# Kernel optimization log

Hardware: AMD Instinct MI355X
Metric: run time of the kernel (lower is better)

Reference implementation:

```python
import jax, jax.numpy as jnp
import numpy as np
import math

# ---- HashGridEncoder constants (from init_kwargs) ----
L = 16            # levels
LOG2T = 19
T = 1 << LOG2T    # hash table size per level
F = 2             # features per entry
N_MIN = 16
N_MAX = 2048
N_PTS = 524288    # number of query points
BB_MIN = np.zeros(3, np.float32)
BB_MAX = np.ones(3, np.float32)
B = math.exp((math.log(N_MAX) - math.log(N_MIN)) / (L - 1))
RES = np.array([math.floor(N_MIN * B ** i) for i in range(L)], dtype=np.float32)  # per-level grid resolution
VERTS = np.array([[0,0,0],[0,0,1],[0,1,0],[0,1,1],[1,0,0],[1,0,1],[1,1,0],[1,1,1]], dtype=np.int32)  # 8 cube corners
PI = np.array([1, 2654435761, 805459861], dtype=np.uint32)  # spatial hash primes
MASK = np.uint32((1 << 19) - 1)  # hard-coded mask from source


def setup_inputs() -> dict:
    key = jax.random.key(0)
    k1, k2 = jax.random.split(key)
    xyz = jax.random.uniform(k1, (N_PTS, 3), dtype=jnp.float32)  # points inside bbox [0,1]^3
    # nn.init.uniform_(weight, -1e-4, 1e-4)
    tables = jax.random.uniform(k2, (L, T, F), minval=-1e-4, maxval=1e-4, dtype=jnp.float32)
    return {"xyz": xyz, "tables": tables}


def reference(xyz, tables):
    # cell size per level: (bb_max - bb_min) / resolution  -> [L,3]
    cell = (BB_MAX - BB_MIN)[None, :] / RES[:, None]
    # normalized grid coords for all levels at once: [L,N,3]
    u = (xyz[None, :, :] - BB_MIN) / cell[:, None, :]
    mi = jnp.floor(u).astype(jnp.int32)            # min corner index [L,N,3]
    d = u - mi.astype(jnp.float32)                 # trilinear fracs == (xyz - min_vertex)/cell, [L,N,3]
    # 8 corner integer coords: [L,N,8,3]; uint32 wrapping matches int64-mul + low-19-bit mask
    corners = (mi[:, :, None, :] + VERTS[None, None]).astype(jnp.uint32)
    h = (corners[..., 0] * PI[0]) ^ (corners[..., 1] * PI[1]) ^ (corners[..., 2] * PI[2])
    h = (h & MASK).astype(jnp.int32)               # hash indices [L,N,8], all < T
    # gather all levels in one flat lookup
    flat = tables.reshape(L * T, F)
    idx = h + (jnp.arange(L, dtype=jnp.int32) * T)[:, None, None]
    emb = flat[idx]                                # [L,N,8,F]
    # trilinear weights: prod over axes of d (corner bit 1) or 1-d (corner bit 0) -> [L,N,8]
    w = jnp.prod(jnp.where(VERTS[None, None].astype(bool), d[:, :, None, :], 1.0 - d[:, :, None, :]), axis=-1)
    c = jnp.einsum('lnv,lnvf->lnf', w, emb)        # interpolated features [L,N,F]
    # torch.cat(embedded, dim=-1): level-major concat -> [N, L*F]
    return jnp.moveaxis(c, 0, 1).reshape(xyz.shape[0], L * F)
```

## Files before the change

kernel.cpp:

```cpp
#include <hip/hip_runtime.h>
#include <cmath>

#define NLEVELS 16
#define TBL     (1u << 19)
#define HMASK   0x7FFFFu
#define NPTS    524288
#define NCHUNK  (NPTS / 256)

typedef float v4f __attribute__((ext_vector_type(4)));

struct LevelParams {
    float cell[NLEVELS];
};

__device__ __forceinline__ float2 level_interp(
    float x, float y, float z, float cell,
    const float2* __restrict__ tab)
{
    const float ux = x / cell;
    const float uy = y / cell;
    const float uz = z / cell;
    const float fx = floorf(ux);
    const float fy = floorf(uy);
    const float fz = floorf(uz);
    const float dx = ux - fx;
    const float dy = uy - fy;
    const float dz = uz - fz;

    const unsigned ix = (unsigned)(int)fx;
    const unsigned iy = (unsigned)(int)fy;
    const unsigned iz = (unsigned)(int)fz;

    const unsigned hx0 = ix;
    const unsigned hx1 = ix + 1u;
    const unsigned hy0 = iy * 2654435761u;
    const unsigned hy1 = (iy + 1u) * 2654435761u;
    const unsigned hz0 = iz * 805459861u;
    const unsigned hz1 = (iz + 1u) * 805459861u;

    const unsigned h0 = (hx0 ^ hy0 ^ hz0) & HMASK;
    const unsigned h1 = (hx0 ^ hy0 ^ hz1) & HMASK;
    const unsigned h2 = (hx0 ^ hy1 ^ hz0) & HMASK;
    const unsigned h3 = (hx0 ^ hy1 ^ hz1) & HMASK;
    const unsigned h4 = (hx1 ^ hy0 ^ hz0) & HMASK;
    const unsigned h5 = (hx1 ^ hy0 ^ hz1) & HMASK;
    const unsigned h6 = (hx1 ^ hy1 ^ hz0) & HMASK;
    const unsigned h7 = (hx1 ^ hy1 ^ hz1) & HMASK;

    const float2 e0 = tab[h0];
    const float2 e1 = tab[h1];
    const float2 e2 = tab[h2];
    const float2 e3 = tab[h3];
    const float2 e4 = tab[h4];
    const float2 e5 = tab[h5];
    const float2 e6 = tab[h6];
    const float2 e7 = tab[h7];

    const float wx0 = 1.0f - dx;
    const float wy0 = 1.0f - dy;
    const float wz0 = 1.0f - dz;

    const float p00 = wx0 * wy0;
    const float p01 = wx0 * dy;
    const float p10 = dx * wy0;
    const float p11 = dx * dy;

    const float w0 = p00 * wz0;
    const float w1 = p00 * dz;
    const float w2 = p01 * wz0;
    const float w3 = p01 * dz;
    const float w4 = p10 * wz0;
    const float w5 = p10 * dz;
    const float w6 = p11 * wz0;
    const float w7 = p11 * dz;

    float c0 = w0 * e0.x;
    float c1 = w0 * e0.y;
    c0 += w1 * e1.x;  c1 += w1 * e1.y;
    c0 += w2 * e2.x;  c1 += w2 * e2.y;
    c0 += w3 * e3.x;  c1 += w3 * e3.y;
    c0 += w4 * e4.x;  c1 += w4 * e4.y;
    c0 += w5 * e5.x;  c1 += w5 * e5.y;
    c0 += w6 * e6.x;  c1 += w6 * e6.y;
    c0 += w7 * e7.x;  c1 += w7 * e7.y;

    return make_float2(c0, c1);
}

__global__ __launch_bounds__(256) void ngp_phase1(
    const float* __restrict__ xyz,
    const float* __restrict__ tables,
    float2* __restrict__ ws,
    LevelParams lp)
{
    const unsigned b = blockIdx.x;
    const int level = (int)(((b >> 14) << 3) | (b & 7u));
    const int chunk = (int)((b >> 3) & (NCHUNK - 1u));
    const int n = chunk * 256 + threadIdx.x;

    const float x = xyz[3 * n + 0];
    const float y = xyz[3 * n + 1];
    const float z = xyz[3 * n + 2];

    const float cell = lp.cell[level];
    const float2* __restrict__ tab = (const float2*)tables + ((size_t)level << 19);

    const float2 c = level_interp(x, y, z, cell, tab);

    ws[(size_t)level * NPTS + n] = c;
}

__global__ __launch_bounds__(256) void ngp_phase2(
    const float2* __restrict__ ws,
    float* __restrict__ out)
{
    const unsigned j = blockIdx.x * 256 + threadIdx.x;
    const unsigned n = j >> 3;
    const unsigned k = j & 7u;

    const float2 a = ws[(size_t)(2u * k)      * NPTS + n];
    const float2 b = ws[(size_t)(2u * k + 1u) * NPTS + n];

    v4f v = { a.x, a.y, b.x, b.y };
    *(v4f*)(out + (size_t)j * 4) = v;
}

__global__ __launch_bounds__(256) void ngp_encode(
    const float* __restrict__ xyz,
    const float* __restrict__ tables,
    float* __restrict__ out,
    LevelParams lp)
{
    const int n = blockIdx.x * 256 + threadIdx.x;
    const float x = xyz[3 * n + 0];
    const float y = xyz[3 * n + 1];
    const float z = xyz[3 * n + 2];

    float acc[2 * NLEVELS];
    const float2* __restrict__ tab_base = (const float2*)tables;

    #pragma unroll
    for (int l = 0; l < NLEVELS; ++l) {
        const float2 c = level_interp(x, y, z, lp.cell[l],
                                      tab_base + ((size_t)l << 19));
        acc[2 * l + 0] = c.x;
        acc[2 * l + 1] = c.y;
    }

    v4f* o4 = (v4f*)(out + (size_t)n * 32);
    #pragma unroll
    for (int j = 0; j < 8; ++j) {
        v4f v = { acc[4 * j + 0], acc[4 * j + 1],
                  acc[4 * j + 2], acc[4 * j + 3] };
        o4[j] = v;
    }
}

extern "C" void kernel_launch(void* const* d_in, const int* in_sizes, int n_in,
                              void* d_out, int out_size, void* d_ws, size_t ws_size,
                              hipStream_t stream) {
    const float* xyz    = (const float*)d_in[0];
    const float* tables = (const float*)d_in[1];
    float* out          = (float*)d_out;

    LevelParams lp;
    const double B = std::exp((std::log(2048.0) - std::log(16.0)) / 15.0);
    for (int i = 0; i < NLEVELS; ++i) {
        const double r = std::floor(16.0 * std::pow(B, (double)i));
        lp.cell[i] = 1.0f / (float)r;
    }

    const size_t ws_needed = (size_t)NLEVELS * NPTS * sizeof(float2);

    if (ws_size >= ws_needed) {
        float2* ws = (float2*)d_ws;
        hipLaunchKernelGGL(ngp_phase1, dim3(NLEVELS * NCHUNK), dim3(256), 0, stream,
                           xyz, tables, ws, lp);
        hipLaunchKernelGGL(ngp_phase2, dim3(NPTS * 8 / 256), dim3(256), 0, stream,
                           ws, out);
    } else {
        hipLaunchKernelGGL(ngp_encode, dim3(NPTS / 256), dim3(256), 0, stream,
                           xyz, tables, out, lp);
    }
}
```

Before: 381.1 us.

## Process two points per thread in phase1 and transpose phase2 via LDS

Phase1 now has each thread handle two points, issuing all 16 gathers before combining, to raise memory-level parallelism and halve the block count. Phase2 stages each block's 256 points times 16 levels in padded shared memory, then writes fully contiguous output rows. This replaces scattered strided reads with coalesced loads. The cost is higher register pressure in phase1 and an LDS round trip plus barrier in phase2.

```diff
diff --git a/kernel.cpp b/kernel.cpp
--- a/kernel.cpp
+++ b/kernel.cpp
@@ -5,7 +5,6 @@
 #define TBL     (1u << 19)
 #define HMASK   0x7FFFFu
 #define NPTS    524288
-#define NCHUNK  (NPTS / 256)
 
 typedef float v4f __attribute__((ext_vector_type(4)));
 
@@ -13,9 +12,9 @@
     float cell[NLEVELS];
 };
 
-__device__ __forceinline__ float2 level_interp(
-    float x, float y, float z, float cell,
-    const float2* __restrict__ tab)
+__device__ __forceinline__ void ngp_hash(
+    float x, float y, float z, float cell, unsigned* __restrict__ h,
+    float& dx, float& dy, float& dz)
 {
     const float ux = x / cell;
     const float uy = y / cell;
@@ -23,9 +22,9 @@
     const float fx = floorf(ux);
     const float fy = floorf(uy);
     const float fz = floorf(uz);
-    const float dx = ux - fx;
-    const float dy = uy - fy;
-    const float dz = uz - fz;
+    dx = ux - fx;
+    dy = uy - fy;
+    dz = uz - fz;
 
     const unsigned ix = (unsigned)(int)fx;
     const unsigned iy = (unsigned)(int)fy;
@@ -38,52 +37,46 @@
     const unsigned hz0 = iz * 805459861u;
     const unsigned hz1 = (iz + 1u) * 805459861u;
 
-    const unsigned h0 = (hx0 ^ hy0 ^ hz0) & HMASK;
-    const unsigned h1 = (hx0 ^ hy0 ^ hz1) & HMASK;
-    const unsigned h2 = (hx0 ^ hy1 ^ hz0) & HMASK;
-    const unsigned h3 = (hx0 ^ hy1 ^ hz1) & HMASK;
-    const unsigned h4 = (hx1 ^ hy0 ^ hz0) & HMASK;
-    const unsigned h5 = (hx1 ^ hy0 ^ hz1) & HMASK;
-    const unsigned h6 = (hx1 ^ hy1 ^ hz0) & HMASK;
-    const unsigned h7 = (hx1 ^ hy1 ^ hz1) & HMASK;
-
-    const float2 e0 = tab[h0];
-    const float2 e1 = tab[h1];
-    const float2 e2 = tab[h2];
-    const float2 e3 = tab[h3];
-    const float2 e4 = tab[h4];
-    const float2 e5 = tab[h5];
-    const float2 e6 = tab[h6];
-    const float2 e7 = tab[h7];
-
+    h[0] = (hx0 ^ hy0 ^ hz0) & HMASK;
+    h[1] = (hx0 ^ hy0 ^ hz1) & HMASK;
+    h[2] = (hx0 ^ hy1 ^ hz0) & HMASK;
+    h[3] = (hx0 ^ hy1 ^ hz1) & HMASK;
+    h[4] = (hx1 ^ hy0 ^ hz0) & HMASK;
+    h[5] = (hx1 ^ hy0 ^ hz1) & HMASK;
+    h[6] = (hx1 ^ hy1 ^ hz0) & HMASK;
+    h[7] = (hx1 ^ hy1 ^ hz1) & HMASK;
+}
+
+__device__ __forceinline__ void ngp_weights(
+    float dx, float dy, float dz, float* __restrict__ w)
+{
     const float wx0 = 1.0f - dx;
     const float wy0 = 1.0f - dy;
     const float wz0 = 1.0f - dz;
-
     const float p00 = wx0 * wy0;
     const float p01 = wx0 * dy;
     const float p10 = dx * wy0;
     const float p11 = dx * dy;
-
-    const float w0 = p00 * wz0;
-    const float w1 = p00 * dz;
-    const float w2 = p01 * wz0;
-    const float w3 = p01 * dz;
-    const float w4 = p10 * wz0;
-    const float w5 = p10 * dz;
-    const float w6 = p11 * wz0;
-    const float w7 = p11 * dz;
-
-    float c0 = w0 * e0.x;
-    float c1 = w0 * e0.y;
-    c0 += w1 * e1.x;  c1 += w1 * e1.y;
-    c0 += w2 * e2.x;  c1 += w2 * e2.y;
-    c0 += w3 * e3.x;  c1 += w3 * e3.y;
-    c0 += w4 * e4.x;  c1 += w4 * e4.y;
-    c0 += w5 * e5.x;  c1 += w5 * e5.y;
-    c0 += w6 * e6.x;  c1 += w6 * e6.y;
-    c0 += w7 * e7.x;  c1 += w7 * e7.y;
-
+    w[0] = p00 * wz0;
+    w[1] = p00 * dz;
+    w[2] = p01 * wz0;
+    w[3] = p01 * dz;
+    w[4] = p10 * wz0;
+    w[5] = p10 * dz;
+    w[6] = p11 * wz0;
+    w[7] = p11 * dz;
+}
+
+__device__ __forceinline__ float2 ngp_combine(
+    const float* __restrict__ w, const float2* __restrict__ e)
+{
+    float c0 = w[0] * e[0].x;
+    float c1 = w[0] * e[0].y;
+    #pragma unroll
+    for (int c = 1; c < 8; ++c) {
+        c0 += w[c] * e[c].x;
+        c1 += w[c] * e[c].y;
+    }
     return make_float2(c0, c1);
 }
 
@@ -94,35 +87,69 @@
     LevelParams lp)
 {
     const unsigned b = blockIdx.x;
-    const int level = (int)(((b >> 14) << 3) | (b & 7u));
-    const int chunk = (int)((b >> 3) & (NCHUNK - 1u));
-    const int n = chunk * 256 + threadIdx.x;
-
-    const float x = xyz[3 * n + 0];
-    const float y = xyz[3 * n + 1];
-    const float z = xyz[3 * n + 2];
+    const int level = (int)(((b >> 13) << 3) | (b & 7u));
+    const int chunk = (int)((b >> 3) & 1023u);
+    const int n0 = chunk * 512 + threadIdx.x;
+    const int n1 = n0 + 256;
+
+    const float x0 = xyz[3 * n0 + 0];
+    const float y0 = xyz[3 * n0 + 1];
+    const float z0 = xyz[3 * n0 + 2];
+    const float x1 = xyz[3 * n1 + 0];
+    const float y1 = xyz[3 * n1 + 1];
+    const float z1 = xyz[3 * n1 + 2];
 
     const float cell = lp.cell[level];
     const float2* __restrict__ tab = (const float2*)tables + ((size_t)level << 19);
 
-    const float2 c = level_interp(x, y, z, cell, tab);
-
-    ws[(size_t)level * NPTS + n] = c;
-}
+    unsigned h0[8], h1[8];
+    float dx0, dy0, dz0, dx1, dy1, dz1;
+    ngp_hash(x0, y0, z0, cell, h0, dx0, dy0, dz0);
+    ngp_hash(x1, y1, z1, cell, h1, dx1, dy1, dz1);
+
+    float2 e0[8], e1[8];
+    #pragma unroll
+    for (int c = 0; c < 8; ++c) e0[c] = tab[h0[c]];
+    #pragma unroll
+    for (int c = 0; c < 8; ++c) e1[c] = tab[h1[c]];
+
+    float w0[8], w1[8];
+    ngp_weights(dx0, dy0, dz0, w0);
+    ngp_weights(dx1, dy1, dz1, w1);
+
+    const float2 r0 = ngp_combine(w0, e0);
+    const float2 r1 = ngp_combine(w1, e1);
+
+    ws[(size_t)level * NPTS + n0] = r0;
+    ws[(size_t)level * NPTS + n1] = r1;
+}
+
+#define P2STRIDE 258
 
 __global__ __launch_bounds__(256) void ngp_phase2(
     const float2* __restrict__ ws,
     float* __restrict__ out)
 {
-    const unsigned j = blockIdx.x * 256 + threadIdx.x;
-    const unsigned n = j >> 3;
-    const unsigned k = j & 7u;
-
-    const float2 a = ws[(size_t)(2u * k)      * NPTS + n];
-    const float2 b = ws[(size_t)(2u * k + 1u) * NPTS + n];
-
-    v4f v = { a.x, a.y, b.x, b.y };
-    *(v4f*)(out + (size_t)j * 4) = v;
+    __shared__ float2 lds[NLEVELS * P2STRIDE];
+    const unsigned base = blockIdx.x * 256;
+    const unsigned tid = threadIdx.x;
+
+    #pragma unroll
+    for (int l = 0; l < NLEVELS; ++l)
+        lds[l * P2STRIDE + tid] = ws[(size_t)l * NPTS + base + tid];
+
+    __syncthreads();
+
+    #pragma unroll
+    for (int it = 0; it < 8; ++it) {
+        const unsigned j = it * 256 + tid;
+        const unsigned nl = j >> 3;
+        const unsigned k = j & 7u;
+        const float2 a = lds[(2u * k)      * P2STRIDE + nl];
+        const float2 b = lds[(2u * k + 1u) * P2STRIDE + nl];
+        v4f v = { a.x, a.y, b.x, b.y };
+        *(v4f*)(out + (size_t)base * 32 + (size_t)j * 4) = v;
+    }
 }
 
 __global__ __launch_bounds__(256) void ngp_encode(
@@ -141,10 +168,18 @@
 
     #pragma unroll
     for (int l = 0; l < NLEVELS; ++l) {
-        const float2 c = level_interp(x, y, z, lp.cell[l],
-                                      tab_base + ((size_t)l << 19));
-        acc[2 * l + 0] = c.x;
-        acc[2 * l + 1] = c.y;
+        unsigned h[8];
+        float dx, dy, dz;
+        ngp_hash(x, y, z, lp.cell[l], h, dx, dy, dz);
+        const float2* __restrict__ tab = tab_base + ((size_t)l << 19);
+        float2 e[8];
+        #pragma unroll
+        for (int c = 0; c < 8; ++c) e[c] = tab[h[c]];
+        float w[8];
+        ngp_weights(dx, dy, dz, w);
+        const float2 r = ngp_combine(w, e);
+        acc[2 * l + 0] = r.x;
+        acc[2 * l + 1] = r.y;
     }
 
     v4f* o4 = (v4f*)(out + (size_t)n * 32);
@@ -174,9 +209,9 @@
 
     if (ws_size >= ws_needed) {
         float2* ws = (float2*)d_ws;
-        hipLaunchKernelGGL(ngp_phase1, dim3(NLEVELS * NCHUNK), dim3(256), 0, stream,
+        hipLaunchKernelGGL(ngp_phase1, dim3(NLEVELS * (NPTS / 512)), dim3(256), 0, stream,
                            xyz, tables, ws, lp);
-        hipLaunchKernelGGL(ngp_phase2, dim3(NPTS * 8 / 256), dim3(256), 0, stream,
+        hipLaunchKernelGGL(ngp_phase2, dim3(NPTS / 256), dim3(256), 0, stream,
                            ws, out);
     } else {
         hipLaunchKernelGGL(ngp_encode, dim3(NPTS / 256), dim3(256), 0, stream,
```

New measurement: 405.0 us. 6.3% more time.
